# Kernel optimization log

Measured on AMD Instinct MI355X. Metric: run time of the kernel, lower is better.

## Reference

```python
import jax, jax.numpy as jnp
import numpy as np

N_NODES = 100000
N_EDGES = 1600000
D_FEAT = 64
D_OUT = 64


def setup_inputs() -> dict:
    key = jax.random.key(0)
    k1, k2, k3, k4 = jax.random.split(key, 4)
    vertices = jax.random.normal(k1, (N_NODES, D_FEAT), dtype=jnp.float32)
    edges = jax.random.randint(k2, (2, N_EDGES), 0, N_NODES, dtype=jnp.int64)
    weight = jax.random.normal(k3, (D_OUT, D_FEAT), dtype=jnp.float32) * (1.0 / np.sqrt(D_FEAT))
    bias = jax.random.normal(k4, (D_OUT,), dtype=jnp.float32) * 0.01
    return {"vertices": vertices, "edges": edges, "weight": weight, "bias": bias}


def reference(vertices, edges, weight, bias):
    # GraphConv forward, dense (non-sparse) path, self_loop=True, normalize=True.
    n_vertices = vertices.shape[0]
    idx = jnp.arange(n_vertices, dtype=edges.dtype)
    dst = jnp.concatenate([edges[0], idx])  # scatter destinations (edges[0])
    src = jnp.concatenate([edges[1], idx])  # gather sources (edges[1])
    # agg[i] = sum over edges with dst==i of vertices[src]
    agg = jax.ops.segment_sum(vertices[src], dst, num_segments=n_vertices)
    # degree per node (torch scatters ones_like(neighbours): all feature cols equal)
    deg = jax.ops.segment_sum(
        jnp.ones_like(dst, dtype=vertices.dtype), dst, num_segments=n_vertices
    )
    agg = agg * (jnp.clip(deg, 1.0, None) ** -0.5)[:, None]
    # Linear: y = agg @ W.T + b
    return agg @ weight.T + bias
```

## Files before the change

kernel.cpp:

```cpp
#include <hip/hip_runtime.h>
#include <hip/hip_fp16.h>

constexpr int N_NODES = 100000;
constexpr int N_EDGES = 1600000;
constexpr int D = 64;

constexpr int SHC    = 9;
constexpr int BSZC   = 1 << SHC;
constexpr int NBC    = (N_NODES + BSZC - 1) / BSZC;
constexpr int SPLITB = 256;
constexpr int TILE   = (N_EDGES + SPLITB - 1) / SPLITB;
constexpr int LINB   = 2048;
constexpr int TILE2  = 8192;
constexpr int NBLK2  = (N_EDGES + TILE2 - 1) / TILE2;

constexpr int SCAN_CHUNK = 1024;
constexpr int NCHUNK = (N_NODES + SCAN_CHUNK - 1) / SCAN_CHUNK;

__device__ __forceinline__ int waveInclScan(int v, int lane) {
    #pragma unroll
    for (int off = 1; off < 64; off <<= 1) {
        int t = __shfl_up(v, off, 64);
        if (lane >= off) v += t;
    }
    return v;
}

__global__ __launch_bounds__(256) void lin_hist(
    const float* __restrict__ vertices,
    const float* __restrict__ weight,
    __half* __restrict__ Yh,
    const int* __restrict__ edges,
    int* __restrict__ bcntC)
{
    if (blockIdx.x < LINB) {
        __shared__ float rowbuf[4][64];
        const int wid  = threadIdx.x >> 6;
        const int lane = threadIdx.x & 63;

        float w[64];
        #pragma unroll
        for (int f = 0; f < 64; ++f) w[f] = weight[lane * 64 + f];

        const int nodesPerIter = LINB * 4;
        for (int base = blockIdx.x * 4; base < N_NODES; base += nodesPerIter) {
            const int node = base + wid;
            float a = 0.0f;
            if (node < N_NODES) a = vertices[(size_t)node * D + lane];
            rowbuf[wid][lane] = a;
            __syncthreads();
            float acc = 0.0f;
            #pragma unroll
            for (int f = 0; f < 64; ++f)
                acc += rowbuf[wid][f] * w[f];
            if (node < N_NODES) Yh[(size_t)node * D + lane] = __float2half(acc);
            __syncthreads();
        }
    } else {
        __shared__ int h[NBC];
        const int b = blockIdx.x - LINB;
        if (threadIdx.x < NBC) h[threadIdx.x] = 0;
        __syncthreads();
        const int lo = b * TILE;
        const int hi = min(lo + TILE, N_EDGES);
        for (int e = lo + threadIdx.x; e < hi; e += 256)
            atomicAdd(&h[edges[e] >> SHC], 1);
        __syncthreads();
        if (threadIdx.x < NBC) {
            int v = h[threadIdx.x];
            if (v) atomicAdd(&bcntC[threadIdx.x], v);
        }
    }
}

__global__ __launch_bounds__(1024) void s_scatter(const int* __restrict__ edges,
                                                  const int* __restrict__ bcntC,
                                                  int* __restrict__ cursorDelta,
                                                  int* __restrict__ bbaseC,
                                                  int* __restrict__ packed)
{
    __shared__ int s[256];
    __shared__ int baseC[NBC];
    __shared__ int h[NBC];
    __shared__ int chunk[NBC];
    const int t = threadIdx.x;

    int v = 0;
    if (t < 256) { v = (t < NBC) ? bcntC[t] : 0; s[t] = v; }
    __syncthreads();
    for (int o = 1; o < 256; o <<= 1) {
        int u = (t < 256 && t >= o) ? s[t - o] : 0;
        __syncthreads();
        if (t < 256) s[t] += u;
        __syncthreads();
    }
    if (t < NBC) {
        int e = s[t] - v;
        baseC[t] = e;
        h[t] = 0;
        if (blockIdx.x == 0) bbaseC[t] = e;
    }
    __syncthreads();

    const int lo = blockIdx.x * TILE2;
    int myd[8];
    #pragma unroll
    for (int k = 0; k < 8; ++k) {
        int e = lo + k * 1024 + t;
        myd[k] = (e < N_EDGES) ? edges[e] : -1;
        if (myd[k] >= 0) atomicAdd(&h[myd[k] >> SHC], 1);
    }
    __syncthreads();

    if (t < NBC) {
        int c = h[t];
        chunk[t] = c ? (baseC[t] + atomicAdd(&cursorDelta[t], c)) : 0;
        h[t] = 0;
    }
    __syncthreads();

    #pragma unroll
    for (int k = 0; k < 8; ++k) {
        if (myd[k] >= 0) {
            int e = lo + k * 1024 + t;
            int src = edges[N_EDGES + e];
            int j = myd[k] >> SHC;
            int r = atomicAdd(&h[j], 1);
            packed[chunk[j] + r] = (src << SHC) | (myd[k] & (BSZC - 1));
        }
    }
}

__global__ __launch_bounds__(1024) void csr512(const int* __restrict__ packed,
                                               const int* __restrict__ bbaseC,
                                               const int* __restrict__ bcntC,
                                               int* __restrict__ offsets,
                                               int* __restrict__ deg,
                                               int* __restrict__ srt)
{
    __shared__ int h2[BSZC];
    __shared__ int cur2[BSZC];
    __shared__ int s[BSZC];
    const int b = blockIdx.x;
    const int t = threadIdx.x;
    const int start = bbaseC[b];
    const int cnt   = bcntC[b];

    if (t < BSZC) h2[t] = 0;
    __syncthreads();
    for (int i = t; i < cnt; i += 1024)
        atomicAdd(&h2[packed[start + i] & (BSZC - 1)], 1);
    __syncthreads();

    if (t < BSZC) s[t] = h2[t];
    __syncthreads();
    for (int o = 1; o < BSZC; o <<= 1) {
        int u = (t < BSZC && t >= o) ? s[t - o] : 0;
        __syncthreads();
        if (t < BSZC) s[t] += u;
        __syncthreads();
    }
    if (t < BSZC) {
        int excl = s[t] - h2[t];
        int node = (b << SHC) + t;
        if (node < N_NODES) { offsets[node] = start + excl; deg[node] = h2[t]; }
        cur2[t] = excl;
    }
    __syncthreads();
    for (int i = t; i < cnt; i += 1024) {
        int p = packed[start + i];
        int r = atomicAdd(&cur2[p & (BSZC - 1)], 1);
        srt[start + r] = p >> SHC;
    }
}

__device__ __forceinline__ void addrow(float* acc, uint4 u)
{
    const __half2* h = reinterpret_cast<const __half2*>(&u);
    #pragma unroll
    for (int k = 0; k < 4; ++k) {
        float2 f = __half22float2(h[k]);
        acc[2 * k]     += f.x;
        acc[2 * k + 1] += f.y;
    }
}

__global__ __launch_bounds__(256) void gather_h(
    const __half* __restrict__ Yh,
    const int* __restrict__ offsets,
    const int* __restrict__ deg,
    const int* __restrict__ srt,
    const float* __restrict__ bias,
    float* __restrict__ out)
{
    const int wid  = threadIdx.x >> 6;
    const int lane = threadIdx.x & 63;
    const int g    = lane >> 3;
    const int sub  = lane & 7;
    const int n0   = blockIdx.x * 8 + wid * 2;
    const int n1   = n0 + 1;
    if (n0 >= N_NODES) return;
    const bool has1 = (n1 < N_NODES);

    const int st0 = offsets[n0];
    const int c0  = deg[n0];
    int st1 = 0, c1 = 0;
    if (has1) { st1 = offsets[n1]; c1 = deg[n1]; }

    float a0[8], a1[8];
    #pragma unroll
    for (int j = 0; j < 8; ++j) { a0[j] = 0.0f; a1[j] = 0.0f; }

    if (g == 0) {
        uint4 u0 = *reinterpret_cast<const uint4*>(Yh + (size_t)n0 * D + sub * 8);
        addrow(a0, u0);
        if (has1) {
            uint4 u1 = *reinterpret_cast<const uint4*>(Yh + (size_t)n1 * D + sub * 8);
            addrow(a1, u1);
        }
    }

    const int m = min(c0 & ~7, c1 & ~7);
    int e = 0;
    for (; e < m; e += 8) {
        int s0 = srt[st0 + e + g];
        int s1 = srt[st1 + e + g];
        uint4 u0 = *reinterpret_cast<const uint4*>(Yh + (size_t)s0 * D + sub * 8);
        uint4 u1 = *reinterpret_cast<const uint4*>(Yh + (size_t)s1 * D + sub * 8);
        addrow(a0, u0);
        addrow(a1, u1);
    }

    int e0 = e;
    for (; e0 + 16 <= c0; e0 += 16) {
        int s0 = srt[st0 + e0 + g];
        int s1 = srt[st0 + e0 + 8 + g];
        uint4 u0 = *reinterpret_cast<const uint4*>(Yh + (size_t)s0 * D + sub * 8);
        uint4 u1 = *reinterpret_cast<const uint4*>(Yh + (size_t)s1 * D + sub * 8);
        addrow(a0, u0);
        addrow(a0, u1);
    }
    if (e0 + 8 <= c0) {
        int s0 = srt[st0 + e0 + g];
        uint4 u0 = *reinterpret_cast<const uint4*>(Yh + (size_t)s0 * D + sub * 8);
        addrow(a0, u0);
        e0 += 8;
    }
    if (e0 + g < c0) {
        int s0 = srt[st0 + e0 + g];
        uint4 u0 = *reinterpret_cast<const uint4*>(Yh + (size_t)s0 * D + sub * 8);
        addrow(a0, u0);
    }

    if (has1) {
        int e1 = e;
        for (; e1 + 16 <= c1; e1 += 16) {
            int s0 = srt[st1 + e1 + g];
            int s1 = srt[st1 + e1 + 8 + g];
            uint4 u0 = *reinterpret_cast<const uint4*>(Yh + (size_t)s0 * D + sub * 8);
            uint4 u1 = *reinterpret_cast<const uint4*>(Yh + (size_t)s1 * D + sub * 8);
            addrow(a1, u0);
            addrow(a1, u1);
        }
        if (e1 + 8 <= c1) {
            int s0 = srt[st1 + e1 + g];
            uint4 u0 = *reinterpret_cast<const uint4*>(Yh + (size_t)s0 * D + sub * 8);
            addrow(a1, u0);
            e1 += 8;
        }
        if (e1 + g < c1) {
            int s0 = srt[st1 + e1 + g];
            uint4 u0 = *reinterpret_cast<const uint4*>(Yh + (size_t)s0 * D + sub * 8);
            addrow(a1, u0);
        }
    }

    #pragma unroll
    for (int j = 0; j < 8; ++j) {
        a0[j] += __shfl_xor(a0[j], 8, 64);
        a0[j] += __shfl_xor(a0[j], 16, 64);
        a0[j] += __shfl_xor(a0[j], 32, 64);
        a1[j] += __shfl_xor(a1[j], 8, 64);
        a1[j] += __shfl_xor(a1[j], 16, 64);
        a1[j] += __shfl_xor(a1[j], 32, 64);
    }

    if (g == 0) {
        const float4 b0 = *reinterpret_cast<const float4*>(bias + sub * 8);
        const float4 b1 = *reinterpret_cast<const float4*>(bias + sub * 8 + 4);
        {
            const float sc = rsqrtf((float)c0 + 1.0f);
            float4 r0, r1;
            r0.x = a0[0] * sc + b0.x;  r0.y = a0[1] * sc + b0.y;
            r0.z = a0[2] * sc + b0.z;  r0.w = a0[3] * sc + b0.w;
            r1.x = a0[4] * sc + b1.x;  r1.y = a0[5] * sc + b1.y;
            r1.z = a0[6] * sc + b1.z;  r1.w = a0[7] * sc + b1.w;
            *reinterpret_cast<float4*>(out + (size_t)n0 * D + sub * 8)     = r0;
            *reinterpret_cast<float4*>(out + (size_t)n0 * D + sub * 8 + 4) = r1;
        }
        if (has1) {
            const float sc = rsqrtf((float)c1 + 1.0f);
            float4 r0, r1;
            r0.x = a1[0] * sc + b0.x;  r0.y = a1[1] * sc + b0.y;
            r0.z = a1[2] * sc + b0.z;  r0.w = a1[3] * sc + b0.w;
            r1.x = a1[4] * sc + b1.x;  r1.y = a1[5] * sc + b1.y;
            r1.z = a1[6] * sc + b1.z;  r1.w = a1[7] * sc + b1.w;
            *reinterpret_cast<float4*>(out + (size_t)n1 * D + sub * 8)     = r0;
            *reinterpret_cast<float4*>(out + (size_t)n1 * D + sub * 8 + 4) = r1;
        }
    }
}


__global__ __launch_bounds__(256) void linear_kernel(
    const float* __restrict__ vertices,
    const float* __restrict__ weight,
    float* __restrict__ Y)
{
    __shared__ float rowbuf[4][64];
    const int wid  = threadIdx.x >> 6;
    const int lane = threadIdx.x & 63;
    float w[64];
    #pragma unroll
    for (int f = 0; f < 64; ++f) w[f] = weight[lane * 64 + f];
    const int nodesPerIter = gridDim.x * 4;
    for (int base = blockIdx.x * 4; base < N_NODES; base += nodesPerIter) {
        const int node = base + wid;
        float a = 0.0f;
        if (node < N_NODES) a = vertices[(size_t)node * D + lane];
        rowbuf[wid][lane] = a;
        __syncthreads();
        float acc = 0.0f;
        #pragma unroll
        for (int f = 0; f < 64; ++f)
            acc += rowbuf[wid][f] * w[f];
        if (node < N_NODES) Y[(size_t)node * D + lane] = acc;
        __syncthreads();
    }
}

__global__ __launch_bounds__(256) void gather_f32(
    const float* __restrict__ Y,
    const int* __restrict__ offsets,
    const int* __restrict__ deg,
    const int* __restrict__ sortedSrc,
    const float* __restrict__ bias,
    float* __restrict__ out)
{
    const int wid  = threadIdx.x >> 6;
    const int lane = threadIdx.x & 63;
    const int g    = lane >> 4;
    const int sub  = lane & 15;
    const int node = blockIdx.x * 4 + wid;
    if (node >= N_NODES) return;

    const int start = offsets[node];
    const int cnt   = deg[node];

    float4 acc;
    if (g == 0) {
        acc = *reinterpret_cast<const float4*>(Y + (size_t)node * D + (sub << 2));
    } else {
        acc.x = 0.0f; acc.y = 0.0f; acc.z = 0.0f; acc.w = 0.0f;
    }

    int e = 0;
    for (; e + 8 <= cnt; e += 8) {
        int s0 = sortedSrc[start + e + g];
        int s1 = sortedSrc[start + e + 4 + g];
        const float4 a0 = *reinterpret_cast<const float4*>(Y + (size_t)s0 * D + (sub << 2));
        const float4 a1 = *reinterpret_cast<const float4*>(Y + (size_t)s1 * D + (sub << 2));
        acc.x += a0.x; acc.y += a0.y; acc.z += a0.z; acc.w += a0.w;
        acc.x += a1.x; acc.y += a1.y; acc.z += a1.z; acc.w += a1.w;
    }
    if (e + 4 <= cnt) {
        int s0 = sortedSrc[start + e + g];
        const float4 a0 = *reinterpret_cast<const float4*>(Y + (size_t)s0 * D + (sub << 2));
        acc.x += a0.x; acc.y += a0.y; acc.z += a0.z; acc.w += a0.w;
        e += 4;
    }
    if (e + g < cnt) {
        int s0 = sortedSrc[start + e + g];
        const float4 a0 = *reinterpret_cast<const float4*>(Y + (size_t)s0 * D + (sub << 2));
        acc.x += a0.x; acc.y += a0.y; acc.z += a0.z; acc.w += a0.w;
    }

    acc.x += __shfl_xor(acc.x, 16, 64);
    acc.y += __shfl_xor(acc.y, 16, 64);
    acc.z += __shfl_xor(acc.z, 16, 64);
    acc.w += __shfl_xor(acc.w, 16, 64);
    acc.x += __shfl_xor(acc.x, 32, 64);
    acc.y += __shfl_xor(acc.y, 32, 64);
    acc.z += __shfl_xor(acc.z, 32, 64);
    acc.w += __shfl_xor(acc.w, 32, 64);

    if (lane < 16) {
        const float sc = rsqrtf((float)cnt + 1.0f);
        const float4 b4 = *reinterpret_cast<const float4*>(bias + (sub << 2));
        float4 r;
        r.x = acc.x * sc + b4.x;
        r.y = acc.y * sc + b4.y;
        r.z = acc.z * sc + b4.z;
        r.w = acc.w * sc + b4.w;
        *reinterpret_cast<float4*>(out + (size_t)node * D + (sub << 2)) = r;
    }
}

__global__ __launch_bounds__(256) void hist_kernel(const int* __restrict__ edges,
                                                   int* __restrict__ deg)
{
    int e = blockIdx.x * 256 + threadIdx.x;
    if (e < N_EDGES) atomicAdd(&deg[edges[e]], 1);
}

__global__ __launch_bounds__(256) void scan_part(const int* __restrict__ deg,
                                                 int* __restrict__ partial)
{
    int t = threadIdx.x;
    int base = blockIdx.x * SCAN_CHUNK + t * 4;
    int s = 0;
    #pragma unroll
    for (int k = 0; k < 4; ++k) { int i = base + k; if (i < N_NODES) s += deg[i]; }
    int lane = t & 63, wid = t >> 6;
    #pragma unroll
    for (int off = 32; off; off >>= 1) s += __shfl_down(s, off, 64);
    __shared__ int red[4];
    if (lane == 0) red[wid] = s;
    __syncthreads();
    if (t == 0) partial[blockIdx.x] = red[0] + red[1] + red[2] + red[3];
}

__global__ void scan_small(int* partial) {
    int lane = threadIdx.x;
    int v0 = (lane < NCHUNK) ? partial[lane] : 0;
    int v1 = (64 + lane < NCHUNK) ? partial[64 + lane] : 0;
    int i0 = waveInclScan(v0, lane);
    int tot0 = __shfl(i0, 63, 64);
    int i1 = waveInclScan(v1, lane) + tot0;
    if (lane < NCHUNK) partial[lane] = i0 - v0;
    if (64 + lane < NCHUNK) partial[64 + lane] = i1 - v1;
}

__global__ __launch_bounds__(256) void scan_final(const int* __restrict__ deg,
                                                  const int* __restrict__ partial,
                                                  int* __restrict__ offsets,
                                                  int* __restrict__ cursor)
{
    int t = threadIdx.x;
    int base = blockIdx.x * SCAN_CHUNK + t * 4;
    int d[4]; int s = 0;
    #pragma unroll
    for (int k = 0; k < 4; ++k) { int i = base + k; d[k] = (i < N_NODES) ? deg[i] : 0; s += d[k]; }
    __shared__ int sd[256];
    sd[t] = s; __syncthreads();
    #pragma unroll
    for (int off = 1; off < 256; off <<= 1) {
        int v = (t >= off) ? sd[t - off] : 0;
        __syncthreads();
        sd[t] += v;
        __syncthreads();
    }
    int excl = sd[t] - s + partial[blockIdx.x];
    #pragma unroll
    for (int k = 0; k < 4; ++k) {
        int i = base + k;
        if (i < N_NODES) { offsets[i] = excl; cursor[i] = excl; excl += d[k]; }
    }
}

__global__ __launch_bounds__(256) void scatter_idx(const int* __restrict__ edges,
                                                   int* __restrict__ cursor,
                                                   int* __restrict__ sortedSrc)
{
    int e = blockIdx.x * 256 + threadIdx.x;
    if (e >= N_EDGES) return;
    int dst = edges[e];
    int src = edges[N_EDGES + e];
    int pos = atomicAdd(&cursor[dst], 1);
    sortedSrc[pos] = src;
}


__global__ __launch_bounds__(256) void fb_scatter(
    const float* __restrict__ vertices, const int* __restrict__ edges,
    float* __restrict__ agg, float* __restrict__ degF)
{
    long long tid = (long long)blockIdx.x * 256 + threadIdx.x;
    int lane = threadIdx.x & 63;
    long long e = tid >> 6;
    if (e >= N_EDGES) return;
    int dst = edges[e];
    int src = edges[N_EDGES + e];
    atomicAdd(&agg[(size_t)dst * D + lane], vertices[(size_t)src * D + lane]);
    if (lane == 0) atomicAdd(&degF[dst], 1.0f);
}

__global__ __launch_bounds__(256) void fb_finish(
    const float* __restrict__ vertices, const float* __restrict__ weight,
    const float* __restrict__ bias, const float* __restrict__ degF,
    float* __restrict__ out)
{
    __shared__ float rowbuf[4][64];
    const int wid  = threadIdx.x >> 6;
    const int lane = threadIdx.x & 63;
    float w[64];
    #pragma unroll
    for (int f = 0; f < 64; ++f) w[f] = weight[lane * 64 + f];
    const float b = bias[lane];
    const int nodesPerIter = gridDim.x * 4;
    for (int base = blockIdx.x * 4; base < N_NODES; base += nodesPerIter) {
        const int node = base + wid;
        float a = 0.0f;
        if (node < N_NODES) {
            const float scale = rsqrtf(degF[node] + 1.0f);
            a = (out[(size_t)node * D + lane] + vertices[(size_t)node * D + lane]) * scale;
        }
        rowbuf[wid][lane] = a;
        __syncthreads();
        float acc = b;
        #pragma unroll
        for (int f = 0; f < 64; ++f) acc += rowbuf[wid][f] * w[f];
        if (node < N_NODES) out[(size_t)node * D + lane] = acc;
        __syncthreads();
    }
}

extern "C" void kernel_launch(void* const* d_in, const int* in_sizes, int n_in,
                              void* d_out, int out_size, void* d_ws, size_t ws_size,
                              hipStream_t stream) {
    const float* vertices = (const float*)d_in[0];
    const int*   edges    = (const int*)d_in[1];
    const float* weight   = (const float*)d_in[2];
    const float* bias     = (const float*)d_in[3];
    float* out = (float*)d_out;

    const int threads = 256;
    const int edgeBlocks = (N_EDGES + threads - 1) / threads;

    {
        __half* Yh         = (__half*)d_ws;
        int*   bcntC       = (int*)(Yh + (size_t)N_NODES * D);
        int*   cursorDelta = bcntC + NBC;
        int*   bbaseC      = cursorDelta + NBC;
        int*   offs        = bbaseC + NBC;
        int*   deg         = offs + N_NODES;
        int*   packed      = deg + N_NODES;
        int*   srt         = packed + N_EDGES;
        size_t needed      = (size_t)((char*)(srt + N_EDGES) - (char*)d_ws);
        if (ws_size >= needed) {
            (void)hipMemsetAsync(bcntC, 0, sizeof(int) * 2 * NBC, stream);
            lin_hist<<<LINB + SPLITB, threads, 0, stream>>>(vertices, weight, Yh, edges, bcntC);
            s_scatter<<<NBLK2, 1024, 0, stream>>>(edges, bcntC, cursorDelta, bbaseC, packed);
            csr512<<<NBC, 1024, 0, stream>>>(packed, bbaseC, bcntC, offs, deg, srt);
            gather_h<<<(N_NODES + 7) / 8, threads, 0, stream>>>(Yh, offs, deg, srt, bias, out);
            return;
        }
    }

    {
        float* Y       = (float*)d_ws;
        int*   deg     = (int*)(Y + (size_t)N_NODES * D);
        int*   offs    = deg + N_NODES;
        int*   cursor  = offs + N_NODES;
        int*   partial = cursor + N_NODES;
        int*   srt     = partial + 128;
        size_t needed  = (size_t)((char*)(srt + N_EDGES) - (char*)d_ws);
        if (ws_size >= needed) {
            (void)hipMemsetAsync(deg, 0, sizeof(int) * N_NODES, stream);
            linear_kernel<<<1024, threads, 0, stream>>>(vertices, weight, Y);
            hist_kernel<<<edgeBlocks, threads, 0, stream>>>(edges, deg);
            scan_part<<<NCHUNK, threads, 0, stream>>>(deg, partial);
            scan_small<<<1, 64, 0, stream>>>(partial);
            scan_final<<<NCHUNK, threads, 0, stream>>>(deg, partial, offs, cursor);
            scatter_idx<<<edgeBlocks, threads, 0, stream>>>(edges, cursor, srt);
            gather_f32<<<(N_NODES + 3) / 4, threads, 0, stream>>>(Y, offs, deg, srt, bias, out);
            return;
        }
    }

    {
        float* degF = (float*)d_ws;
        (void)hipMemsetAsync(out, 0, sizeof(float) * (size_t)N_NODES * D, stream);
        (void)hipMemsetAsync(degF, 0, sizeof(float) * N_NODES, stream);
        const long long totalScatter = (long long)N_EDGES * 64;
        fb_scatter<<<(int)((totalScatter + threads - 1) / threads), threads, 0, stream>>>(
            vertices, edges, out, degF);
        fb_finish<<<1024, threads, 0, stream>>>(vertices, weight, bias, degF, out);
    }
}
```

Measured before the change: 117.5 us.

## Compute linear projection with fp16 MFMA tiles instead of scalar FMA loop

Replaces the scalar per-lane dot-product linear stage (each lane holding a 64-float weight row, with shared-memory row broadcast and barriers) with 16x16x32 fp16 MFMA instructions. Each wave processes a 16-node tile, converting vertex and weight fragments to fp16 in registers. This removes the register-heavy, barrier-bound FMA loop, at the cost of fp16 rounding of inputs and weights before accumulation. The fused histogram blocks are unchanged.

Result: faster. 107.5 us (-8.5%).

```diff
diff --git a/kernel.cpp b/kernel.cpp
--- a/kernel.cpp
+++ b/kernel.cpp
@@ -4,13 +4,17 @@
 constexpr int N_NODES = 100000;
 constexpr int N_EDGES = 1600000;
 constexpr int D = 64;
+
+typedef _Float16 half8 __attribute__((ext_vector_type(8)));
+typedef float floatx4 __attribute__((ext_vector_type(4)));
 
 constexpr int SHC    = 9;
 constexpr int BSZC   = 1 << SHC;
 constexpr int NBC    = (N_NODES + BSZC - 1) / BSZC;
 constexpr int SPLITB = 256;
 constexpr int TILE   = (N_EDGES + SPLITB - 1) / SPLITB;
-constexpr int LINB   = 2048;
+constexpr int NTILES = N_NODES / 16;
+constexpr int MFB    = (NTILES + 3) / 4;
 constexpr int TILE2  = 8192;
 constexpr int NBLK2  = (N_EDGES + TILE2 - 1) / TILE2;
 
@@ -26,39 +30,74 @@
     return v;
 }
 
-__global__ __launch_bounds__(256) void lin_hist(
+__global__ __launch_bounds__(256) void mfma_hist(
     const float* __restrict__ vertices,
     const float* __restrict__ weight,
     __half* __restrict__ Yh,
     const int* __restrict__ edges,
     int* __restrict__ bcntC)
 {
-    if (blockIdx.x < LINB) {
-        __shared__ float rowbuf[4][64];
+    if (blockIdx.x < MFB) {
         const int wid  = threadIdx.x >> 6;
         const int lane = threadIdx.x & 63;
-
-        float w[64];
+        const int tile = blockIdx.x * 4 + wid;
+        if (tile >= NTILES) return;
+
+        const int row16 = lane & 15;
+        const int kgrp  = lane >> 4;
+
+        half8 bfrag[2][4];
         #pragma unroll
-        for (int f = 0; f < 64; ++f) w[f] = weight[lane * 64 + f];
-
-        const int nodesPerIter = LINB * 4;
-        for (int base = blockIdx.x * 4; base < N_NODES; base += nodesPerIter) {
-            const int node = base + wid;
-            float a = 0.0f;
-            if (node < N_NODES) a = vertices[(size_t)node * D + lane];
-            rowbuf[wid][lane] = a;
-            __syncthreads();
-            float acc = 0.0f;
+        for (int c = 0; c < 2; ++c) {
             #pragma unroll
-            for (int f = 0; f < 64; ++f)
-                acc += rowbuf[wid][f] * w[f];
-            if (node < N_NODES) Yh[(size_t)node * D + lane] = __float2half(acc);
-            __syncthreads();
+            for (int jg = 0; jg < 4; ++jg) {
+                const float* wp = weight + (size_t)(jg * 16 + row16) * 64 + c * 32 + kgrp * 8;
+                float4 w0 = *reinterpret_cast<const float4*>(wp);
+                float4 w1 = *reinterpret_cast<const float4*>(wp + 4);
+                half8 h;
+                h[0] = (_Float16)w0.x; h[1] = (_Float16)w0.y;
+                h[2] = (_Float16)w0.z; h[3] = (_Float16)w0.w;
+                h[4] = (_Float16)w1.x; h[5] = (_Float16)w1.y;
+                h[6] = (_Float16)w1.z; h[7] = (_Float16)w1.w;
+                bfrag[c][jg] = h;
+            }
+        }
+
+        const int base = tile * 16;
+        half8 afrag[2];
+        #pragma unroll
+        for (int c = 0; c < 2; ++c) {
+            const float* xp = vertices + (size_t)(base + row16) * 64 + c * 32 + kgrp * 8;
+            float4 x0 = *reinterpret_cast<const float4*>(xp);
+            float4 x1 = *reinterpret_cast<const float4*>(xp + 4);
+            half8 h;
+            h[0] = (_Float16)x0.x; h[1] = (_Float16)x0.y;
+            h[2] = (_Float16)x0.z; h[3] = (_Float16)x0.w;
+            h[4] = (_Float16)x1.x; h[5] = (_Float16)x1.y;
+            h[6] = (_Float16)x1.z; h[7] = (_Float16)x1.w;
+            afrag[c] = h;
+        }
+
+        floatx4 acc[4];
+        #pragma unroll
+        for (int jg = 0; jg < 4; ++jg) {
+            floatx4 a = {0.0f, 0.0f, 0.0f, 0.0f};
+            a = __builtin_amdgcn_mfma_f32_16x16x32_f16(afrag[0], bfrag[0][jg], a, 0, 0, 0);
+            a = __builtin_amdgcn_mfma_f32_16x16x32_f16(afrag[1], bfrag[1][jg], a, 0, 0, 0);
+            acc[jg] = a;
+        }
+
+        #pragma unroll
+        for (int jg = 0; jg < 4; ++jg) {
+            #pragma unroll
+            for (int r = 0; r < 4; ++r) {
+                const int node = base + kgrp * 4 + r;
+                Yh[(size_t)node * 64 + jg * 16 + row16] = __float2half(acc[jg][r]);
+            }
         }
     } else {
         __shared__ int h[NBC];
-        const int b = blockIdx.x - LINB;
+        const int b = blockIdx.x - MFB;
         if (threadIdx.x < NBC) h[threadIdx.x] = 0;
         __syncthreads();
         const int lo = b * TILE;
@@ -549,7 +588,7 @@
         size_t needed      = (size_t)((char*)(srt + N_EDGES) - (char*)d_ws);
         if (ws_size >= needed) {
             (void)hipMemsetAsync(bcntC, 0, sizeof(int) * 2 * NBC, stream);
-            lin_hist<<<LINB + SPLITB, threads, 0, stream>>>(vertices, weight, Yh, edges, bcntC);
+            mfma_hist<<<MFB + SPLITB, threads, 0, stream>>>(vertices, weight, Yh, edges, bcntC);
             s_scatter<<<NBLK2, 1024, 0, stream>>>(edges, bcntC, cursorDelta, bbaseC, packed);
             csr512<<<NBC, 1024, 0, stream>>>(packed, bbaseC, bcntC, offs, deg, srt);
             gather_h<<<(N_NODES + 7) / 8, threads, 0, stream>>>(Yh, offs, deg, srt, bias, out);
```
